# Optimization experiments

Hardware: AMD Instinct MI355X
Metric: run time of the kernel (lower is better)

## Reference

```python
import jax, jax.numpy as jnp
import numpy as np

N_NODES = 50000
N_EDGES = 800000
F_DIM = 64


def setup_inputs() -> dict:
    key = jax.random.key(0)
    ks = jax.random.split(key, 11)
    inp = {
        "x": jax.random.normal(ks[0], (1,), dtype=jnp.float32),  # unused by the module
        "features": jax.random.normal(ks[1], (N_NODES, F_DIM), dtype=jnp.float32),
        "edge_index": jax.random.randint(ks[2], (2, N_EDGES), 0, N_NODES, dtype=jnp.int64),
        # Conv2d(1, 8, (2,1)) -> weight (8,1,2,1) flattened to (8,2)
        "conv_w": jax.random.normal(ks[3], (8, 2), dtype=jnp.float32) * (1.0 / np.sqrt(2.0)),
        "conv_b": jax.random.normal(ks[4], (8,), dtype=jnp.float32) * 0.1,
        "w1": jax.random.normal(ks[5], (16, F_DIM), dtype=jnp.float32) * (1.0 / np.sqrt(F_DIM)),
        "b1": jax.random.normal(ks[6], (16,), dtype=jnp.float32) * 0.1,
        "w2": jax.random.normal(ks[7], (1, 16), dtype=jnp.float32) * (1.0 / np.sqrt(16.0)),
        "b2": jax.random.normal(ks[8], (1,), dtype=jnp.float32) * 0.1,
        "w3": jax.random.normal(ks[9], (1, 8), dtype=jnp.float32) * (1.0 / np.sqrt(8.0)),
        "b3": jax.random.normal(ks[10], (1,), dtype=jnp.float32) * 0.1,
    }
    return inp


def reference(x, features, edge_index, conv_w, conv_b, w1, b1, w2, b2, w3, b3):
    # Gather endpoint features for each edge: (E, F) each
    src, dst = edge_index[0], edge_index[1]
    f1 = features[src]
    f2 = features[dst]
    # Conv2d(1,8,(2,1)) on (E,1,2,F) collapses the 2-row stack:
    # out[e,o,f] = w[o,0]*f1[e,f] + w[o,1]*f2[e,f] + b[o]
    feat = (f1[:, None, :] * conv_w[None, :, 0, None]
            + f2[:, None, :] * conv_w[None, :, 1, None]
            + conv_b[None, :, None])          # (E, 8, F)
    feat = jax.nn.relu(feat)
    # fc1: Linear(F, 16) applied over last dim -> (E, 8, 16)
    feat = jax.nn.relu(jnp.einsum('eof,gf->eog', feat, w1) + b1)
    # fc2: Linear(16, 1) -> (E, 8, 1) -> reshape (E, 8)
    feat = jax.nn.relu(jnp.einsum('eog,hg->eoh', feat, w2) + b2)
    feat = feat.reshape(-1, 8)
    # fc3: Linear(8, 1) + sigmoid -> (E, 1)
    out = jax.nn.sigmoid(feat @ w3.T + b3)
    return out
```

## Files before the change

### kernel.cpp

```cpp
#include <hip/hip_runtime.h>
#include <hip/hip_bf16.h>


typedef _Float16 f16x8 __attribute__((ext_vector_type(8)));
typedef _Float16 f16x4 __attribute__((ext_vector_type(4)));
typedef _Float16 f16x2 __attribute__((ext_vector_type(2)));
typedef short    bf16x8 __attribute__((ext_vector_type(8)));
typedef float    f32x4  __attribute__((ext_vector_type(4)));
typedef float    f32x2  __attribute__((ext_vector_type(2)));

union U8 { f16x8 v; f16x2 p[4]; };

static __device__ __forceinline__ short f2bf(float f) {
    union { __hip_bfloat16 h; short s; } u;
    u.h = __float2bfloat16(f);
    return u.s;
}

__global__ __launch_bounds__(256) void feat_to_f16(const float* __restrict__ in,
                                                   _Float16* __restrict__ out,
                                                   int n4) {
    int i = blockIdx.x * blockDim.x + threadIdx.x;
    const int stride = gridDim.x * blockDim.x;
    for (; i < n4; i += stride) {
        const f32x4 v = ((const f32x4*)in)[i];
        ((f16x4*)out)[i] = __builtin_convertvector(v, f16x4);
    }
}

__global__ __launch_bounds__(256, 4) void edgeconv_f16_x4(
    const _Float16* __restrict__ feat16,
    const int*      __restrict__ edge_index,
    const float* __restrict__ conv_w, const float* __restrict__ conv_b,
    const float* __restrict__ w1,     const float* __restrict__ b1,
    const float* __restrict__ w2,     const float* __restrict__ b2,
    const float* __restrict__ w3,     const float* __restrict__ b3,
    float* __restrict__ out, int nEdges)
{
    const int tid = threadIdx.x;
    const int l   = tid & 63;
    const int wid = tid >> 6;
    const int grp = l >> 4;
    const int n   = l & 15;
    const int ch  = l & 7;
    const int el  = (l >> 3) & 1;

    const float* w1r = w1 + n * 64 + grp * 8;
    f16x8 aw0, aw1;
    #pragma unroll
    for (int i = 0; i < 8; ++i) {
        aw0[i] = (_Float16)w1r[i];
        aw1[i] = (_Float16)w1r[32 + i];
    }

    const _Float16 cah = (_Float16)conv_w[2 * ch];
    const _Float16 cch = (_Float16)conv_w[2 * ch + 1];
    const _Float16 cbh = (_Float16)conv_b[ch];
    const f16x2 vca = {cah, cah}, vcc = {cch, cch}, vcb = {cbh, cbh};
    const f16x2 vzero = {(_Float16)0.f, (_Float16)0.f};

    f32x4 accInit;
    float w2r[4];
    #pragma unroll
    for (int r = 0; r < 4; ++r) {
        accInit[r] = b1[grp * 4 + r];
        w2r[r]     = w2[grp * 4 + r];
    }
    const float w3v = w3[ch];
    const float b2v = b2[0];
    const float b3v = b3[0];

    const int nGroups    = (nEdges + 15) >> 4;
    const int totalWaves = gridDim.x * 4;
    int g = blockIdx.x * 4 + wid;
    if (g >= nGroups) return;

#define LOADT(VS, VD, T, SLo, SHi, DLo, DHi) do { \
    const int sn_ = __shfl((VS), 2 * (T) + el); \
    const int dn_ = __shfl((VD), 2 * (T) + el); \
    const _Float16* ps_ = feat16 + (size_t)sn_ * 64 + grp * 8; \
    const _Float16* pd_ = feat16 + (size_t)dn_ * 64 + grp * 8; \
    SLo = *(const f16x8*)(ps_);  SHi = *(const f16x8*)(ps_ + 32); \
    DLo = *(const f16x8*)(pd_);  DHi = *(const f16x8*)(pd_ + 32); \
} while (0)

    int ce = min(g * 16 + n, nEdges - 1);
    int vs = edge_index[ce];
    int vd = edge_index[nEdges + ce];

    f16x8 sL[2], sH[2], dL[2], dH[2];
    LOADT(vs, vd, 0, sL[0], sH[0], dL[0], dH[0]);
    LOADT(vs, vd, 1, sL[1], sH[1], dL[1], dH[1]);

    while (true) {
        const int gn    = g + totalWaves;
        const bool more = (gn < nGroups);
        int vsn = 0, vdn = 0;
        if (more) {
            const int cen = min(gn * 16 + n, nEdges - 1);
            vsn = edge_index[cen];
            vdn = edge_index[nEdges + cen];
        }

        float zp[8];
        #pragma unroll
        for (int t = 0; t < 8; ++t) {
            const int b = t & 1;

            U8 s0_, s1_, d0_, d1_, c0, c1;
            s0_.v = sL[b]; s1_.v = sH[b];
            d0_.v = dL[b]; d1_.v = dH[b];
            #pragma unroll
            for (int p = 0; p < 4; ++p) {
                f16x2 tL = __builtin_elementwise_fma(vca, s0_.p[p],
                            __builtin_elementwise_fma(vcc, d0_.p[p], vcb));
                c0.p[p] = __builtin_elementwise_max(tL, vzero);
                f16x2 tH = __builtin_elementwise_fma(vca, s1_.p[p],
                            __builtin_elementwise_fma(vcc, d1_.p[p], vcb));
                c1.p[p] = __builtin_elementwise_max(tH, vzero);
            }

            if (t < 6)      LOADT(vs,  vd,  t + 2, sL[b], sH[b], dL[b], dH[b]);
            else if (more)  LOADT(vsn, vdn, t - 6, sL[b], sH[b], dL[b], dH[b]);

            f32x4 acc = accInit;
            acc = __builtin_amdgcn_mfma_f32_16x16x32_f16(aw0, c0.v, acc, 0, 0, 0);
            acc = __builtin_amdgcn_mfma_f32_16x16x32_f16(aw1, c1.v, acc, 0, 0, 0);

            float z_ = 0.f;
            #pragma unroll
            for (int r = 0; r < 4; ++r) {
                const float h1 = fmaxf(acc[r], 0.f);
                z_ = fmaf(h1, w2r[r], z_);
            }
            zp[t] = z_;
        }

        #pragma unroll
        for (int t = 0; t < 8; ++t) zp[t] += __shfl_xor(zp[t], 16);
        #pragma unroll
        for (int t = 0; t < 8; ++t) zp[t] += __shfl_xor(zp[t], 32);
        #pragma unroll
        for (int t = 0; t < 8; ++t) {
            const float h2 = fmaxf(zp[t] + b2v, 0.f);
            zp[t] = h2 * w3v;
        }
        #pragma unroll
        for (int t = 0; t < 8; ++t) zp[t] += __shfl_xor(zp[t], 1);
        #pragma unroll
        for (int t = 0; t < 8; ++t) zp[t] += __shfl_xor(zp[t], 2);
        #pragma unroll
        for (int t = 0; t < 8; ++t) zp[t] += __shfl_xor(zp[t], 4);
        #pragma unroll
        for (int t = 0; t < 8; ++t) {
            const float z  = zp[t] + b3v;
            const float sg = 1.0f / (1.0f + __expf(-z));
            if ((l & 55) == 0) {
                const int e = g * 16 + 2 * t + (l >> 3);
                if (e < nEdges) out[e] = sg;
            }
        }

        if (!more) break;
        g = gn; vs = vsn; vd = vdn;
    }
#undef LOADT
}

__global__ __launch_bounds__(256) void edgeconv_mfma2(
    const float* __restrict__ features, const int* __restrict__ edge_index,
    const float* __restrict__ conv_w, const float* __restrict__ conv_b,
    const float* __restrict__ w1, const float* __restrict__ b1,
    const float* __restrict__ w2, const float* __restrict__ b2,
    const float* __restrict__ w3, const float* __restrict__ b3,
    float* __restrict__ out, int nEdges)
{
    const int tid = threadIdx.x;
    const int l   = tid & 63;
    const int wid = tid >> 6;
    const int grp = l >> 4;
    const int n   = l & 15;
    const int ch  = l & 7;
    const int el  = (l >> 3) & 1;

    const float* w1r = w1 + n * 64 + grp * 8;
    bf16x8 aw0, aw1;
    #pragma unroll
    for (int i = 0; i < 8; ++i) {
        aw0[i] = f2bf(w1r[i]);
        aw1[i] = f2bf(w1r[32 + i]);
    }
    const float ca = conv_w[2 * ch];
    const float cc = conv_w[2 * ch + 1];
    const float cb = conv_b[ch];
    float b1r[4], w2r[4];
    #pragma unroll
    for (int r = 0; r < 4; ++r) { b1r[r] = b1[grp * 4 + r]; w2r[r] = w2[grp * 4 + r]; }
    const float w3v = w3[ch];
    const float b2v = b2[0];
    const float b3v = b3[0];

    const int ebase = (blockIdx.x * 4 + wid) * 16;
    const int ce    = min(ebase + n, nEdges - 1);
    const int vs    = edge_index[ce];
    const int vd    = edge_index[nEdges + ce];

#define LOAD_TILE4(T, X1, X2) do { \
    const int sn_ = __shfl(vs, 2 * (T) + el); \
    const int dn_ = __shfl(vd, 2 * (T) + el); \
    const float* p1_ = features + (size_t)sn_ * 64 + grp * 8; \
    const float* p2_ = features + (size_t)dn_ * 64 + grp * 8; \
    X1[0] = *(const f32x4*)(p1_);      X1[1] = *(const f32x4*)(p1_ + 4); \
    X1[2] = *(const f32x4*)(p1_ + 32); X1[3] = *(const f32x4*)(p1_ + 36); \
    X2[0] = *(const f32x4*)(p2_);      X2[1] = *(const f32x4*)(p2_ + 4); \
    X2[2] = *(const f32x4*)(p2_ + 32); X2[3] = *(const f32x4*)(p2_ + 36); \
} while (0)

    f32x4 x1v[4], x2v[4];
    LOAD_TILE4(0, x1v, x2v);
    const f32x2 vca = {ca, ca}, vcc = {cc, cc}, vcb = {cb, cb};
    const f32x2 vz  = {0.f, 0.f};

    #pragma unroll
    for (int t = 0; t < 8; ++t) {
        f32x4 n1v[4], n2v[4];
        if (t < 7) LOAD_TILE4(t + 1, n1v, n2v);
        bf16x8 cf0, cf1;
        #pragma unroll
        for (int p = 0; p < 8; ++p) {
            const int q = p >> 1;
            const int o = (p & 1) * 2;
            f32x2 u = {x1v[q][o], x1v[q][o + 1]};
            f32x2 v = {x2v[q][o], x2v[q][o + 1]};
            f32x2 tt = __builtin_elementwise_fma(vca, u,
                        __builtin_elementwise_fma(vcc, v, vcb));
            tt = __builtin_elementwise_max(tt, vz);
            const short s0 = f2bf(tt[0]), s1 = f2bf(tt[1]);
            if (p < 4) { cf0[2 * (p & 3)] = s0; cf0[2 * (p & 3) + 1] = s1; }
            else       { cf1[2 * (p & 3)] = s0; cf1[2 * (p & 3) + 1] = s1; }
        }
        f32x4 acc = {0.f, 0.f, 0.f, 0.f};
        acc = __builtin_amdgcn_mfma_f32_16x16x32_bf16(aw0, cf0, acc, 0, 0, 0);
        acc = __builtin_amdgcn_mfma_f32_16x16x32_bf16(aw1, cf1, acc, 0, 0, 0);
        float zp = 0.f;
        #pragma unroll
        for (int r = 0; r < 4; ++r) {
            const float h1 = fmaxf(acc[r] + b1r[r], 0.f);
            zp = fmaf(h1, w2r[r], zp);
        }
        zp += __shfl_xor(zp, 16);
        zp += __shfl_xor(zp, 32);
        const float h2 = fmaxf(zp + b2v, 0.f);
        float t3 = h2 * w3v;
        t3 += __shfl_xor(t3, 1);
        t3 += __shfl_xor(t3, 2);
        t3 += __shfl_xor(t3, 4);
        const float z  = t3 + b3v;
        const float sg = 1.0f / (1.0f + __expf(-z));
        if ((l & 55) == 0) {
            const int e = ebase + 2 * t + (l >> 3);
            if (e < nEdges) out[e] = sg;
        }
        if (t < 7) {
            #pragma unroll
            for (int i = 0; i < 4; ++i) { x1v[i] = n1v[i]; x2v[i] = n2v[i]; }
        }
    }
#undef LOAD_TILE4
}

extern "C" void kernel_launch(void* const* d_in, const int* in_sizes, int n_in,
                              void* d_out, int out_size, void* d_ws, size_t ws_size,
                              hipStream_t stream) {
    const float* features = (const float*)d_in[1];
    const int*   edge_idx = (const int*)d_in[2];
    const float* conv_w   = (const float*)d_in[3];
    const float* conv_b   = (const float*)d_in[4];
    const float* w1       = (const float*)d_in[5];
    const float* b1       = (const float*)d_in[6];
    const float* w2       = (const float*)d_in[7];
    const float* b2       = (const float*)d_in[8];
    const float* w3       = (const float*)d_in[9];
    const float* b3       = (const float*)d_in[10];
    float*       out      = (float*)d_out;

    const int nEdges = in_sizes[2] / 2;
    const int nFeat  = in_sizes[1];

    const size_t need = (size_t)nFeat * sizeof(_Float16);
    if (ws_size >= need) {
        _Float16* feat16 = (_Float16*)d_ws;
        feat_to_f16<<<2048, 256, 0, stream>>>(features, feat16, nFeat / 4);
        const int nGroups = (nEdges + 15) >> 4;
        const int blocks  = min(2048, (nGroups + 3) / 4);
        edgeconv_f16_x4<<<blocks, 256, 0, stream>>>(feat16, edge_idx,
                                                    conv_w, conv_b, w1, b1, w2, b2, w3, b3,
                                                    out, nEdges);
    } else {
        const dim3 grid((nEdges + 63) / 64);
        edgeconv_mfma2<<<grid, 256, 0, stream>>>(features, edge_idx,
                                                 conv_w, conv_b, w1, b1, w2, b2, w3, b3,
                                                 out, nEdges);
    }
}
```

Before: 84.81 us.

## Gather edge features via direct global-to-LDS loads with staged waitcnt

Measured after the change: 130.0 us. +53.3%, slower.

```diff
diff --git a/kernel.cpp b/kernel.cpp
--- a/kernel.cpp
+++ b/kernel.cpp
@@ -8,6 +8,12 @@
 typedef short    bf16x8 __attribute__((ext_vector_type(8)));
 typedef float    f32x4  __attribute__((ext_vector_type(4)));
 typedef float    f32x2  __attribute__((ext_vector_type(2)));
+
+#if defined(__has_builtin)
+#if __has_builtin(__builtin_amdgcn_global_load_lds)
+#define HAS_GLDS 1
+#endif
+#endif
 
 union U8 { f16x8 v; f16x2 p[4]; };
 
@@ -28,7 +34,8 @@
     }
 }
 
-__global__ __launch_bounds__(256, 4) void edgeconv_f16_x4(
+#ifdef HAS_GLDS
+__global__ __launch_bounds__(256, 8) void edgeconv_f16_glds(
     const _Float16* __restrict__ feat16,
     const int*      __restrict__ edge_index,
     const float* __restrict__ conv_w, const float* __restrict__ conv_b,
@@ -37,6 +44,8 @@
     const float* __restrict__ w3,     const float* __restrict__ b3,
     float* __restrict__ out, int nEdges)
 {
+    __shared__ __align__(16) char smem[4][4][1024];
+
     const int tid = threadIdx.x;
     const int l   = tid & 63;
     const int wid = tid >> 6;
@@ -44,6 +53,10 @@
     const int n   = l & 15;
     const int ch  = l & 7;
     const int el  = (l >> 3) & 1;
+    const int chunk = l & 7;
+    const int rr    = l >> 3;
+    const int eloc  = rr >> 1;
+    const int endp  = rr & 1;
 
     const float* w1r = w1 + n * 64 + grp * 8;
     f16x8 aw0, aw1;
@@ -75,24 +88,26 @@
     int g = blockIdx.x * 4 + wid;
     if (g >= nGroups) return;
 
-#define LOADT(VS, VD, T, SLo, SHi, DLo, DHi) do { \
-    const int sn_ = __shfl((VS), 2 * (T) + el); \
-    const int dn_ = __shfl((VD), 2 * (T) + el); \
-    const _Float16* ps_ = feat16 + (size_t)sn_ * 64 + grp * 8; \
-    const _Float16* pd_ = feat16 + (size_t)dn_ * 64 + grp * 8; \
-    SLo = *(const f16x8*)(ps_);  SHi = *(const f16x8*)(ps_ + 32); \
-    DLo = *(const f16x8*)(pd_);  DHi = *(const f16x8*)(pd_ + 32); \
-} while (0)
-
     int ce = min(g * 16 + n, nEdges - 1);
     int vs = edge_index[ce];
     int vd = edge_index[nEdges + ce];
 
-    f16x8 sL[2], sH[2], dL[2], dH[2];
-    LOADT(vs, vd, 0, sL[0], sH[0], dL[0], dH[0]);
-    LOADT(vs, vd, 1, sL[1], sH[1], dL[1], dH[1]);
+    char* myLds = (char*)&smem[wid][0][0];
 
     while (true) {
+        #pragma unroll
+        for (int p = 0; p < 4; ++p) {
+            const int si  = __shfl(vs, 4 * p + eloc);
+            const int di  = __shfl(vd, 4 * p + eloc);
+            const int idx = endp ? di : si;
+            const char* ga = (const char*)feat16
+                           + (size_t)(unsigned)idx * 128u + chunk * 16;
+            __builtin_amdgcn_global_load_lds(
+                (const __attribute__((address_space(1))) void*)ga,
+                (__attribute__((address_space(3))) void*)(myLds + p * 1024),
+                16, 0, 0);
+        }
+
         const int gn    = g + totalWaves;
         const bool more = (gn < nGroups);
         int vsn = 0, vdn = 0;
@@ -104,36 +119,45 @@
 
         float zp[8];
         #pragma unroll
-        for (int t = 0; t < 8; ++t) {
-            const int b = t & 1;
-
-            U8 s0_, s1_, d0_, d1_, c0, c1;
-            s0_.v = sL[b]; s1_.v = sH[b];
-            d0_.v = dL[b]; d1_.v = dH[b];
+        for (int p = 0; p < 4; ++p) {
+            if      (p == 0) asm volatile("s_waitcnt vmcnt(3)" ::: "memory");
+            else if (p == 1) asm volatile("s_waitcnt vmcnt(2)" ::: "memory");
+            else if (p == 2) asm volatile("s_waitcnt vmcnt(1)" ::: "memory");
+            else             asm volatile("s_waitcnt vmcnt(0)" ::: "memory");
+            __builtin_amdgcn_sched_barrier(0);
+
+            const char* pb = myLds + p * 1024;
             #pragma unroll
-            for (int p = 0; p < 4; ++p) {
-                f16x2 tL = __builtin_elementwise_fma(vca, s0_.p[p],
-                            __builtin_elementwise_fma(vcc, d0_.p[p], vcb));
-                c0.p[p] = __builtin_elementwise_max(tL, vzero);
-                f16x2 tH = __builtin_elementwise_fma(vca, s1_.p[p],
-                            __builtin_elementwise_fma(vcc, d1_.p[p], vcb));
-                c1.p[p] = __builtin_elementwise_max(tH, vzero);
+            for (int q = 0; q < 2; ++q) {
+                const int roff = q * 512 + el * 256 + grp * 16;
+                U8 s0_, s1_, d0_, d1_, c0, c1;
+                s0_.v = *(const f16x8*)(pb + roff);
+                s1_.v = *(const f16x8*)(pb + roff + 64);
+                d0_.v = *(const f16x8*)(pb + roff + 128);
+                d1_.v = *(const f16x8*)(pb + roff + 192);
+
+                #pragma unroll
+                for (int pp = 0; pp < 4; ++pp) {
+                    f16x2 tL = __builtin_elementwise_fma(vca, s0_.p[pp],
+                                __builtin_elementwise_fma(vcc, d0_.p[pp], vcb));
+                    c0.p[pp] = __builtin_elementwise_max(tL, vzero);
+                    f16x2 tH = __builtin_elementwise_fma(vca, s1_.p[pp],
+                                __builtin_elementwise_fma(vcc, d1_.p[pp], vcb));
+                    c1.p[pp] = __builtin_elementwise_max(tH, vzero);
+                }
+
+                f32x4 acc = accInit;
+                acc = __builtin_amdgcn_mfma_f32_16x16x32_f16(aw0, c0.v, acc, 0, 0, 0);
+                acc = __builtin_amdgcn_mfma_f32_16x16x32_f16(aw1, c1.v, acc, 0, 0, 0);
+
+                float z_ = 0.f;
+                #pragma unroll
+                for (int r = 0; r < 4; ++r) {
+                    const float h1 = fmaxf(acc[r], 0.f);
+                    z_ = fmaf(h1, w2r[r], z_);
+                }
+                zp[2 * p + q] = z_;
             }
-
-            if (t < 6)      LOADT(vs,  vd,  t + 2, sL[b], sH[b], dL[b], dH[b]);
-            else if (more)  LOADT(vsn, vdn, t - 6, sL[b], sH[b], dL[b], dH[b]);
-
-            f32x4 acc = accInit;
-            acc = __builtin_amdgcn_mfma_f32_16x16x32_f16(aw0, c0.v, acc, 0, 0, 0);
-            acc = __builtin_amdgcn_mfma_f32_16x16x32_f16(aw1, c1.v, acc, 0, 0, 0);
-
-            float z_ = 0.f;
-            #pragma unroll
-            for (int r = 0; r < 4; ++r) {
-                const float h1 = fmaxf(acc[r], 0.f);
-                z_ = fmaf(h1, w2r[r], z_);
-            }
-            zp[t] = z_;
         }
 
         #pragma unroll
@@ -164,8 +188,8 @@
         if (!more) break;
         g = gn; vs = vsn; vd = vdn;
     }
-#undef LOADT
-}
+}
+#endif
 
 __global__ __launch_bounds__(256) void edgeconv_mfma2(
     const float* __restrict__ features, const int* __restrict__ edge_index,
@@ -288,18 +312,20 @@
     const int nFeat  = in_sizes[1];
 
     const size_t need = (size_t)nFeat * sizeof(_Float16);
+#ifdef HAS_GLDS
     if (ws_size >= need) {
         _Float16* feat16 = (_Float16*)d_ws;
         feat_to_f16<<<2048, 256, 0, stream>>>(features, feat16, nFeat / 4);
         const int nGroups = (nEdges + 15) >> 4;
         const int blocks  = min(2048, (nGroups + 3) / 4);
-        edgeconv_f16_x4<<<blocks, 256, 0, stream>>>(feat16, edge_idx,
-                                                    conv_w, conv_b, w1, b1, w2, b2, w3, b3,
-                                                    out, nEdges);
-    } else {
-        const dim3 grid((nEdges + 63) / 64);
-        edgeconv_mfma2<<<grid, 256, 0, stream>>>(features, edge_idx,
-                                                 conv_w, conv_b, w1, b1, w2, b2, w3, b3,
-                                                 out, nEdges);
-    }
-}
+        edgeconv_f16_glds<<<blocks, 256, 0, stream>>>(feat16, edge_idx,
+                                                      conv_w, conv_b, w1, b1, w2, b2, w3, b3,
+                                                      out, nEdges);
+        return;
+    }
+#endif
+    const dim3 grid((nEdges + 63) / 64);
+    edgeconv_mfma2<<<grid, 256, 0, stream>>>(features, edge_idx,
+                                             conv_w, conv_b, w1, b1, w2, b2, w3, b3,
+                                             out, nEdges);
+}
```
